# Kernel tuning notes

Measured on AMD Instinct MI355X. Metric: run time of the kernel, lower is better.

Reference implementation:

```python
import jax, jax.numpy as jnp
import numpy as np

B, C, N, K, O = 8, 64, 4096, 20, 64
EPS = 1e-5


def setup_inputs() -> dict:
    key = jax.random.key(0)
    k1, k2, k3 = jax.random.split(key, 3)
    x = jax.random.normal(k1, (B, C, N), dtype=jnp.float32)
    # Conv2d(2C, O, kernel_size=1) -> weight [O, 2C], bias [O]
    fan_in = 2 * C
    bound = 1.0 / np.sqrt(fan_in)
    W = jax.random.uniform(k2, (O, 2 * C), minval=-bound, maxval=bound, dtype=jnp.float32)
    b = jax.random.uniform(k3, (O,), minval=-bound, maxval=bound, dtype=jnp.float32)
    gamma = jnp.ones((O,), dtype=jnp.float32)
    beta = jnp.zeros((O,), dtype=jnp.float32)
    return {"x": x, "W": W, "b": b, "gamma": gamma, "beta": beta}


def reference(x, W, b, gamma, beta):
    k = K
    Bs, Cs, Ns = x.shape
    x_t = jnp.transpose(x, (0, 2, 1))  # [B, N, C]
    # pairwise squared distances (monotonic with cdist, same topk indices)
    sq = jnp.sum(x_t * x_t, axis=-1)  # [B, N]
    d2 = sq[:, :, None] + sq[:, None, :] - 2.0 * jnp.einsum("bnc,bmc->bnm", x_t, x_t)
    valid_k = min(k, Ns - 1)
    _, idx = jax.lax.top_k(-d2, valid_k + 1)  # smallest distances
    idx = idx[:, :, 1:]  # drop self -> [B, N, k]
    # gather neighbor features per batch
    nbr = jax.vmap(lambda xt, i: xt[i])(x_t, idx)  # [B, N, k, C]
    central = x_t[:, :, None, :]  # [B, N, 1, C]
    edge = jnp.concatenate(
        [jnp.broadcast_to(central, (Bs, Ns, k, Cs)), nbr - central], axis=-1
    )  # [B, N, k, 2C]
    # 1x1 conv == channel matmul
    y = jnp.einsum("bnkc,oc->bonk", edge, W) + b[None, :, None, None]  # [B, O, N, k]
    # BatchNorm2d in training mode: batch statistics over (B, N, k)
    mean = jnp.mean(y, axis=(0, 2, 3), keepdims=True)
    var = jnp.var(y, axis=(0, 2, 3), keepdims=True)
    yn = (y - mean) * jax.lax.rsqrt(var + EPS)
    yn = gamma[None, :, None, None] * yn + beta[None, :, None, None]
    out = jax.nn.relu(yn)
    return jnp.max(out, axis=-1)  # [B, O, N]
```

## Files before the change

### kernel.cpp

```cpp
#include <hip/hip_runtime.h>
#include <hip/hip_bf16.h>

#define BB 8
#define CC 64
#define NN 4096
#define KK 20
#define OO 64
#define FMAXV 3.402823466e38f

typedef __attribute__((ext_vector_type(8))) short short8;
typedef __attribute__((ext_vector_type(4))) float f32x4;

__global__ __launch_bounds__(256) void kprep(const float* __restrict__ x,
                                             const float* __restrict__ W,
                                             const float* __restrict__ bias,
                                             float* __restrict__ xt,
                                             unsigned short* __restrict__ xb,
                                             float* __restrict__ sq,
                                             float* __restrict__ u,
                                             float* __restrict__ v) {
  __shared__ float tile[64][65];
  const int b = blockIdx.y, n0 = blockIdx.x * 64;
  const int lane = threadIdx.x & 63, grp = threadIdx.x >> 6;
  #pragma unroll
  for (int j = 0; j < 16; ++j) {
    int c = grp + j * 4;
    tile[c][lane] = x[((size_t)b * CC + c) * NN + n0 + lane];
  }
  float w2r[64], wdr[64];
  const float4* W4 = (const float4*)W;
  #pragma unroll
  for (int c4 = 0; c4 < 16; ++c4) {
    float4 q1 = W4[lane * 32 + c4];
    float4 q2 = W4[lane * 32 + 16 + c4];
    w2r[c4*4]=q2.x; w2r[c4*4+1]=q2.y; w2r[c4*4+2]=q2.z; w2r[c4*4+3]=q2.w;
    wdr[c4*4]=q1.x-q2.x; wdr[c4*4+1]=q1.y-q2.y; wdr[c4*4+2]=q1.z-q2.z; wdr[c4*4+3]=q1.w-q2.w;
  }
  const float bo = bias[lane];
  __syncthreads();
  #pragma unroll
  for (int j = 0; j < 16; ++j) {
    int n = grp + j * 4;
    float vv = tile[lane][n];
    size_t off = ((size_t)b * NN + n0 + n) * CC + lane;
    xt[off] = vv;
    unsigned int uu = __builtin_bit_cast(unsigned int, vv);
    xb[off] = (unsigned short)((uu + 0x7FFFu + ((uu >> 16) & 1u)) >> 16);
  }
  if (threadIdx.x < 64) {
    float s = 0.f;
    #pragma unroll
    for (int c = 0; c < 64; ++c) { float vv = tile[c][lane]; s += vv * vv; }
    sq[(size_t)b * NN + n0 + lane] = s;
  }
  for (int j = 0; j < 16; ++j) {
    int nl = grp * 16 + j;
    float du = 0.f, dv = 0.f;
    #pragma unroll
    for (int c = 0; c < 64; ++c) {
      float xv = tile[c][nl];
      du += w2r[c] * xv;
      dv += wdr[c] * xv;
    }
    size_t off = ((size_t)b * NN + n0 + nl) * OO + lane;
    u[off] = du;
    v[off] = dv + bo;
  }
}

__device__ __forceinline__ int lanes_below(unsigned long long m) {
  unsigned lo = (unsigned)m, hi = (unsigned)(m >> 32);
  int c = __builtin_amdgcn_mbcnt_lo(lo, 0);
  return (int)__builtin_amdgcn_mbcnt_hi(hi, (unsigned)c);
}

__device__ __forceinline__ unsigned packkey(float d, int m) {
  unsigned u = __builtin_bit_cast(unsigned, d);
  u ^= ((int)u < 0) ? 0xFFFFFFFFu : 0x80000000u;
  return (u & 0xFFFFF000u) | (unsigned)m;
}

__device__ __forceinline__ float unpackkey(unsigned t) {
  unsigned u = t | 0xFFFu;
  u = (u & 0x80000000u) ? (u ^ 0x80000000u) : ~u;
  return __builtin_bit_cast(float, u);
}

__device__ __forceinline__ unsigned bitonic64(unsigned v, int lane) {
  #pragma unroll
  for (int k = 2; k <= 64; k <<= 1) {
    #pragma unroll
    for (int j = k >> 1; j >= 1; j >>= 1) {
      unsigned o = (unsigned)__shfl_xor((int)v, j);
      bool up    = ((lane & k) == 0);
      bool lower = ((lane & j) == 0);
      unsigned mn = (v < o) ? v : o;
      unsigned mx = (v < o) ? o : v;
      v = (up == lower) ? mn : mx;
    }
  }
  return v;
}

__global__ __launch_bounds__(256, 4) void kknn6(const unsigned short* __restrict__ xb,
                                                const float* __restrict__ sq,
                                                unsigned* __restrict__ kcand) {
  __shared__ unsigned slist[4][16][32];
  __shared__ unsigned sbuf[4][16][64];
  const int lane = threadIdx.x & 63, w = threadIdx.x >> 6;
  const int wid = blockIdx.x * 4 + w;
  const int b = wid >> 9;
  const int half = (wid >> 8) & 1;
  const int n0g = (wid & 255) * 16;
  const int ch0 = half * (NN / 2);
  const int l15 = lane & 15, q = lane >> 4;
  const unsigned long long qmask = 0xFFFFull << (q * 16);

  const unsigned short* xbB = xb + (size_t)b * NN * CC;
  const float* sqB = sq + (size_t)b * NN;

  #pragma unroll
  for (int i = 0; i < 8; ++i) {
    int idx = i * 64 + lane;
    slist[w][idx >> 5][idx & 31] = 0xFFFFFFFFu;
  }

  short8 afr[2];
  #pragma unroll
  for (int ks = 0; ks < 2; ++ks)
    afr[ks] = __builtin_bit_cast(short8, *(const int4*)(xbB + (size_t)(n0g + l15) * CC + ks * 32 + q * 8));

  float tauf4[4];
  int cnt4[4], done4[4];
  #pragma unroll
  for (int j = 0; j < 4; ++j) { tauf4[j] = FMAXV; cnt4[j] = 0; done4[j] = 0; }

  for (int t = 0; t < 32; ++t) {
    const int cb = ch0 + t * 64;
    short8 bfr[4][2];
    float sv[4];
    #pragma unroll
    for (int ct = 0; ct < 4; ++ct) {
      #pragma unroll
      for (int ks = 0; ks < 2; ++ks)
        bfr[ct][ks] = __builtin_bit_cast(short8,
            *(const int4*)(xbB + (size_t)(cb + ct * 16 + l15) * CC + ks * 32 + q * 8));
      sv[ct] = sqB[cb + ct * 16 + l15];
    }
    f32x4 acc[4];
    #pragma unroll
    for (int ct = 0; ct < 4; ++ct) {
      acc[ct] = (f32x4){0.f, 0.f, 0.f, 0.f};
      acc[ct] = __builtin_amdgcn_mfma_f32_16x16x32_bf16(afr[0], bfr[ct][0], acc[ct], 0, 0, 0);
      acc[ct] = __builtin_amdgcn_mfma_f32_16x16x32_bf16(afr[1], bfr[ct][1], acc[ct], 0, 0, 0);
    }

    #pragma unroll
    for (int ct = 0; ct < 4; ++ct) {
      const int colg = cb + ct * 16 + l15;
      float dj[4];
      bool pj[4];
      #pragma unroll
      for (int j = 0; j < 4; ++j) {
        float d = sv[ct] - 2.f * acc[ct][j];
        if (colg == n0g + q * 4 + j) d = FMAXV;
        dj[j] = d;
        pj[j] = d <= tauf4[j];
      }
      if (!__ballot(pj[0] | pj[1] | pj[2] | pj[3])) continue;
      #pragma unroll
      for (int j = 0; j < 4; ++j) {
        unsigned long long bal = __ballot(pj[j]);
        if (!bal) continue;
        const int rowl = q * 4 + j;
        int posq = lanes_below(bal & qmask);
        if (pj[j]) sbuf[w][rowl][(cnt4[j] + posq) & 63] = packkey(dj[j], colg);
        cnt4[j] += __popcll(bal & qmask);
        unsigned long long mb = __ballot(cnt4[j] - done4[j] >= 32);
        while (mb) {
          int src = __ffsll(mb) - 1;
          int qm = src >> 4;
          int rowm = qm * 4 + j;
          int dsrc = __shfl(done4[j], src);
          unsigned v = (lane < 32) ? slist[w][rowm][lane]
                                   : sbuf[w][rowm][(dsrc + lane - 32) & 63];
          v = bitonic64(v, lane);
          if (lane < 32) slist[w][rowm][lane] = v;
          unsigned tn = (unsigned)__shfl((int)v, 31);
          if (q == qm) { tauf4[j] = unpackkey(tn); done4[j] += 32; }
          mb &= ~(0xFFFFull << (qm * 16));
        }
      }
    }
  }

  #pragma unroll
  for (int j = 0; j < 4; ++j) {
    unsigned long long mb = __ballot(cnt4[j] > done4[j]);
    while (mb) {
      int src = __ffsll(mb) - 1;
      int qm = src >> 4;
      int rowm = qm * 4 + j;
      int dsrc = __shfl(done4[j], src);
      int csrc = __shfl(cnt4[j], src);
      int rem = csrc - dsrc;
      unsigned v = (lane < 32) ? slist[w][rowm][lane]
                 : ((lane - 32) < rem ? sbuf[w][rowm][(dsrc + lane - 32) & 63] : 0xFFFFFFFFu);
      v = bitonic64(v, lane);
      if (lane < 32) slist[w][rowm][lane] = v;
      if (q == qm) done4[j] = cnt4[j];
      mb &= ~(0xFFFFull << (qm * 16));
    }
  }

  unsigned* kc = kcand + (((size_t)b * 2 + half) * NN + n0g) * 32;
  #pragma unroll
  for (int i = 0; i < 8; ++i) {
    int idx = i * 64 + lane;
    kc[idx] = slist[w][idx >> 5][idx & 31];
  }
}

__global__ __launch_bounds__(256) void kpost(const unsigned* __restrict__ kcand,
                                             const float* __restrict__ xt,
                                             const float* __restrict__ sq,
                                             const float* __restrict__ u,
                                             const float* __restrict__ v,
                                             float* __restrict__ umax,
                                             float* __restrict__ umin,
                                             float* __restrict__ gS) {
  const int lane = threadIdx.x & 63, w = threadIdx.x >> 6;
  const int gw = blockIdx.x * 4 + w;
  const int hl = lane & 31;
  float s1 = 0.f, s2 = 0.f;

  for (int it = 0; it < 2; ++it) {
    const int rbase = gw * 4 + it * 2;
    const int b = rbase >> 12;
    const int n = rbase & (NN - 1);

    const unsigned* kc0 = kcand + (((size_t)b * 2 + 0) * NN) * 32;
    const unsigned* kc1 = kcand + (((size_t)b * 2 + 1) * NN) * 32;
    unsigned vA = (lane < 32) ? kc0[(size_t)n * 32 + lane] : kc1[(size_t)n * 32 + (lane - 32)];
    vA = bitonic64(vA, lane);
    unsigned vB = (lane < 32) ? kc0[(size_t)(n + 1) * 32 + lane] : kc1[(size_t)(n + 1) * 32 + (lane - 32)];
    vB = bitonic64(vB, lane);
    unsigned kx = (unsigned)__shfl_xor((int)vB, 32);
    unsigned key = (lane < 32) ? vA : kx;
    int m = (int)(key & 0xFFFu);
    const int rowg = n + ((lane >= 32) ? 1 : 0);

    const float* xtB = xt + (size_t)b * NN * CC;
    const float* sqB = sq + (size_t)b * NN;
    const float4* pr = (const float4*)(xtB + (size_t)rowg * CC);
    const float4* pm = (const float4*)(xtB + (size_t)m * CC);
    float t0 = 0.f, t1 = 0.f, t2 = 0.f, t3 = 0.f;
    #pragma unroll
    for (int i = 0; i < 16; ++i) {
      float4 a = pr[i], c = pm[i];
      t0 += a.x * c.x; t1 += a.y * c.y; t2 += a.z * c.z; t3 += a.w * c.w;
    }
    float ev = sqB[m] - 2.f * ((t0 + t1) + (t2 + t3));

    #pragma unroll
    for (int k = 2; k <= 32; k <<= 1) {
      #pragma unroll
      for (int jj = k >> 1; jj >= 1; jj >>= 1) {
        float e2 = __shfl_xor(ev, jj);
        int   m2 = __shfl_xor(m, jj);
        bool up    = ((hl & k) == 0);
        bool lower = ((hl & jj) == 0);
        bool less  = (e2 < ev) || (e2 == ev && m2 < m);
        bool take  = (up == lower) ? less : !less;
        if (take) { ev = e2; m = m2; }
      }
    }

    const float* uB = u + (size_t)b * NN * OO;
    #pragma unroll
    for (int rr = 0; rr < 2; ++rr) {
      const int rown = n + rr;
      float vv = v[((size_t)b * NN + rown) * OO + lane];
      float mx = -FMAXV, mn = FMAXV;
      #pragma unroll
      for (int k = 0; k < KK; ++k) {
        int id = __shfl(m, rr * 32 + k);
        float uu = uB[(size_t)id * OO + lane];
        float y = vv + uu;
        s1 += y; s2 += y * y;
        mx = fmaxf(mx, uu); mn = fminf(mn, uu);
      }
      umax[((size_t)b * NN + rown) * OO + lane] = mx;
      umin[((size_t)b * NN + rown) * OO + lane] = mn;
    }
  }

  __shared__ float r1[4][64], r2[4][64];
  r1[w][lane] = s1; r2[w][lane] = s2;
  __syncthreads();
  if (w == 0) {
    float a = r1[0][lane] + r1[1][lane] + r1[2][lane] + r1[3][lane];
    float c = r2[0][lane] + r2[1][lane] + r2[2][lane] + r2[3][lane];
    float* g = gS + (blockIdx.x & 7) * 128;
    atomicAdd(&g[lane], a);
    atomicAdd(&g[64 + lane], c);
  }
}

__global__ __launch_bounds__(256) void kout(const float* __restrict__ v,
                                            const float* __restrict__ umax,
                                            const float* __restrict__ umin,
                                            const float* __restrict__ gS,
                                            const float* __restrict__ gamma,
                                            const float* __restrict__ beta,
                                            float* __restrict__ out) {
  __shared__ float sA[64], sB[64];
  __shared__ float zt[64][65];
  const int b = blockIdx.y, n0 = blockIdx.x * 64;
  const int lane = threadIdx.x & 63, w = threadIdx.x >> 6;
  if (threadIdx.x < 64) {
    float s1 = 0.f, s2 = 0.f;
    #pragma unroll
    for (int rsub = 0; rsub < 8; ++rsub) {
      s1 += gS[rsub * 128 + lane];
      s2 += gS[rsub * 128 + 64 + lane];
    }
    const float cnt = (float)BB * NN * KK;
    float m  = s1 / cnt;
    float var = s2 / cnt - m * m;
    float A = gamma[lane] * rsqrtf(var + 1e-5f);
    sA[lane] = A;
    sB[lane] = beta[lane] - A * m;
  }
  __syncthreads();
  for (int j = 0; j < 16; ++j) {
    int nl = w * 16 + j;
    size_t off = ((size_t)b * NN + n0 + nl) * OO + lane;
    float A = sA[lane];
    float c0 = A * v[off] + sB[lane];
    float z = c0 + A * ((A > 0.f) ? umax[off] : umin[off]);
    zt[nl][lane] = fmaxf(z, 0.f);
  }
  __syncthreads();
  for (int j = 0; j < 16; ++j) {
    int o = w * 16 + j;
    out[((size_t)b * OO + o) * NN + n0 + lane] = zt[lane][o];
  }
}

extern "C" void kernel_launch(void* const* d_in, const int* in_sizes, int n_in,
                              void* d_out, int out_size, void* d_ws, size_t ws_size,
                              hipStream_t stream) {
  const float* x     = (const float*)d_in[0];
  const float* W     = (const float*)d_in[1];
  const float* bias  = (const float*)d_in[2];
  const float* gamma = (const float*)d_in[3];
  const float* beta  = (const float*)d_in[4];
  float* out = (float*)d_out;

  float* xt  = (float*)d_ws;
  float* sq  = xt  + (size_t)BB*NN*CC;
  float* u   = sq  + (size_t)BB*NN;
  float* v   = u   + (size_t)BB*NN*OO;
  float* umx = v   + (size_t)BB*NN*OO;
  float* umn = umx + (size_t)BB*NN*OO;
  float* gS  = umn + (size_t)BB*NN*OO;
  unsigned short* xb = (unsigned short*)(gS + 1024);
  unsigned* kcand = (unsigned*)(xb + (size_t)BB*NN*CC);

  hipMemsetAsync(gS, 0, 1024 * sizeof(float), stream);
  kprep<<<dim3(NN/64, BB), 256, 0, stream>>>(x, W, bias, xt, xb, sq, u, v);
  kknn6<<<dim3(1024),      256, 0, stream>>>(xb, sq, kcand);
  kpost<<<dim3(2048),      256, 0, stream>>>(kcand, xt, sq, u, v, umx, umn, gS);
  kout <<<dim3(NN/64, BB), 256, 0, stream>>>(v, umx, umn, gS, gamma, beta, out);
}
```

Baseline: 417.0 us.

## Double-buffer kNN candidate tile loads and pair bitonic merges across row groups

```diff
diff --git a/kernel.cpp b/kernel.cpp
--- a/kernel.cpp
+++ b/kernel.cpp
@@ -102,9 +102,9 @@
   return v;
 }
 
-__global__ __launch_bounds__(256, 4) void kknn6(const unsigned short* __restrict__ xb,
-                                                const float* __restrict__ sq,
-                                                unsigned* __restrict__ kcand) {
+__global__ __launch_bounds__(256, 4) void kknn6c(const unsigned short* __restrict__ xb,
+                                                 const float* __restrict__ sq,
+                                                 unsigned* __restrict__ kcand) {
   __shared__ unsigned slist[4][16][32];
   __shared__ unsigned sbuf[4][16][64];
   const int lane = threadIdx.x & 63, w = threadIdx.x >> 6;
@@ -135,25 +135,32 @@
   #pragma unroll
   for (int j = 0; j < 4; ++j) { tauf4[j] = FMAXV; cnt4[j] = 0; done4[j] = 0; }
 
-  for (int t = 0; t < 32; ++t) {
+  short8 bfr[2][4][2];
+  float sv[2][4];
+  auto loadB = [&](int t, int buf) {
     const int cb = ch0 + t * 64;
-    short8 bfr[4][2];
-    float sv[4];
     #pragma unroll
     for (int ct = 0; ct < 4; ++ct) {
       #pragma unroll
       for (int ks = 0; ks < 2; ++ks)
-        bfr[ct][ks] = __builtin_bit_cast(short8,
+        bfr[buf][ct][ks] = __builtin_bit_cast(short8,
             *(const int4*)(xbB + (size_t)(cb + ct * 16 + l15) * CC + ks * 32 + q * 8));
-      sv[ct] = sqB[cb + ct * 16 + l15];
-    }
+      sv[buf][ct] = sqB[cb + ct * 16 + l15];
+    }
+  };
+  loadB(0, 0);
+
+  for (int t = 0; t < 32; ++t) {
+    const int cb = ch0 + t * 64;
+    const int cur = t & 1;
     f32x4 acc[4];
     #pragma unroll
     for (int ct = 0; ct < 4; ++ct) {
       acc[ct] = (f32x4){0.f, 0.f, 0.f, 0.f};
-      acc[ct] = __builtin_amdgcn_mfma_f32_16x16x32_bf16(afr[0], bfr[ct][0], acc[ct], 0, 0, 0);
-      acc[ct] = __builtin_amdgcn_mfma_f32_16x16x32_bf16(afr[1], bfr[ct][1], acc[ct], 0, 0, 0);
-    }
+      acc[ct] = __builtin_amdgcn_mfma_f32_16x16x32_bf16(afr[0], bfr[cur][ct][0], acc[ct], 0, 0, 0);
+      acc[ct] = __builtin_amdgcn_mfma_f32_16x16x32_bf16(afr[1], bfr[cur][ct][1], acc[ct], 0, 0, 0);
+    }
+    if (t < 31) loadB(t + 1, cur ^ 1);
 
     #pragma unroll
     for (int ct = 0; ct < 4; ++ct) {
@@ -162,7 +169,7 @@
       bool pj[4];
       #pragma unroll
       for (int j = 0; j < 4; ++j) {
-        float d = sv[ct] - 2.f * acc[ct][j];
+        float d = sv[cur][ct] - 2.f * acc[ct][j];
         if (colg == n0g + q * 4 + j) d = FMAXV;
         dj[j] = d;
         pj[j] = d <= tauf4[j];
@@ -178,17 +185,52 @@
         cnt4[j] += __popcll(bal & qmask);
         unsigned long long mb = __ballot(cnt4[j] - done4[j] >= 32);
         while (mb) {
-          int src = __ffsll(mb) - 1;
-          int qm = src >> 4;
-          int rowm = qm * 4 + j;
-          int dsrc = __shfl(done4[j], src);
-          unsigned v = (lane < 32) ? slist[w][rowm][lane]
-                                   : sbuf[w][rowm][(dsrc + lane - 32) & 63];
-          v = bitonic64(v, lane);
-          if (lane < 32) slist[w][rowm][lane] = v;
-          unsigned tn = (unsigned)__shfl((int)v, 31);
-          if (q == qm) { tauf4[j] = unpackkey(tn); done4[j] += 32; }
-          mb &= ~(0xFFFFull << (qm * 16));
+          int src0 = __ffsll(mb) - 1;
+          int qm0 = src0 >> 4;
+          mb &= ~(0xFFFFull << (qm0 * 16));
+          if (mb) {
+            int src1 = __ffsll(mb) - 1;
+            int qm1 = src1 >> 4;
+            mb &= ~(0xFFFFull << (qm1 * 16));
+            const int rowm0 = qm0 * 4 + j, rowm1 = qm1 * 4 + j;
+            int d0 = __shfl(done4[j], qm0 * 16);
+            int d1 = __shfl(done4[j], qm1 * 16);
+            unsigned v0 = (lane < 32) ? slist[w][rowm0][lane]
+                                      : sbuf[w][rowm0][(d0 + lane - 32) & 63];
+            unsigned v1 = (lane < 32) ? slist[w][rowm1][lane]
+                                      : sbuf[w][rowm1][(d1 + lane - 32) & 63];
+            #pragma unroll
+            for (int k = 2; k <= 64; k <<= 1) {
+              #pragma unroll
+              for (int jj = k >> 1; jj >= 1; jj >>= 1) {
+                const bool up    = ((lane & k) == 0);
+                const bool lower = ((lane & jj) == 0);
+                unsigned o0 = (unsigned)__shfl_xor((int)v0, jj);
+                unsigned o1 = (unsigned)__shfl_xor((int)v1, jj);
+                unsigned mn0 = (v0 < o0) ? v0 : o0, mx0 = (v0 < o0) ? o0 : v0;
+                unsigned mn1 = (v1 < o1) ? v1 : o1, mx1 = (v1 < o1) ? o1 : v1;
+                v0 = (up == lower) ? mn0 : mx0;
+                v1 = (up == lower) ? mn1 : mx1;
+              }
+            }
+            if (lane < 32) {
+              slist[w][rowm0][lane] = v0;
+              slist[w][rowm1][lane] = v1;
+            }
+            unsigned tn0 = (unsigned)__shfl((int)v0, 31);
+            unsigned tn1 = (unsigned)__shfl((int)v1, 31);
+            if (q == qm0) { tauf4[j] = unpackkey(tn0); done4[j] += 32; }
+            if (q == qm1) { tauf4[j] = unpackkey(tn1); done4[j] += 32; }
+          } else {
+            const int rowm = qm0 * 4 + j;
+            int dsrc = __shfl(done4[j], qm0 * 16);
+            unsigned v = (lane < 32) ? slist[w][rowm][lane]
+                                     : sbuf[w][rowm][(dsrc + lane - 32) & 63];
+            v = bitonic64(v, lane);
+            if (lane < 32) slist[w][rowm][lane] = v;
+            unsigned tn = (unsigned)__shfl((int)v, 31);
+            if (q == qm0) { tauf4[j] = unpackkey(tn); done4[j] += 32; }
+          }
         }
       }
     }
@@ -369,8 +411,8 @@
   unsigned* kcand = (unsigned*)(xb + (size_t)BB*NN*CC);
 
   hipMemsetAsync(gS, 0, 1024 * sizeof(float), stream);
-  kprep<<<dim3(NN/64, BB), 256, 0, stream>>>(x, W, bias, xt, xb, sq, u, v);
-  kknn6<<<dim3(1024),      256, 0, stream>>>(xb, sq, kcand);
-  kpost<<<dim3(2048),      256, 0, stream>>>(kcand, xt, sq, u, v, umx, umn, gS);
-  kout <<<dim3(NN/64, BB), 256, 0, stream>>>(v, umx, umn, gS, gamma, beta, out);
-}
+  kprep <<<dim3(NN/64, BB), 256, 0, stream>>>(x, W, bias, xt, xb, sq, u, v);
+  kknn6c<<<dim3(1024),      256, 0, stream>>>(xb, sq, kcand);
+  kpost <<<dim3(2048),      256, 0, stream>>>(kcand, xt, sq, u, v, umx, umn, gS);
+  kout  <<<dim3(NN/64, BB), 256, 0, stream>>>(v, umx, umn, gS, gamma, beta, out);
+}
```

New measurement: 590.5 us. 41.6% more time.
